# Kernel optimization log

Hardware: AMD Instinct MI355X
Metric: run time of the kernel (lower is better)

The kernel has to match this reference:

```python
import jax, jax.numpy as jnp
import numpy as np

DIM = 1024
HEADS = 16
HEAD_DIM = DIM // HEADS
SCALE = HEAD_DIM ** -0.5


def setup_inputs() -> dict:
    key = jax.random.key(0)
    ks = jax.random.split(key, 8)
    B, Nx, N, C = 4, 2048, 512, DIM
    s = C ** -0.5
    return {
        "x": jax.random.normal(ks[0], (B, Nx, C), jnp.float32),
        "cls": jax.random.normal(ks[1], (B, N, C), jnp.float32),
        # Linear weights stored as [in, out] (y = x @ W); qkv_bias=False so no biases on kv/q/Lin_att
        "w_kv": jax.random.normal(ks[2], (C, 2 * C), jnp.float32) * s,
        "w_q": jax.random.normal(ks[3], (C, C), jnp.float32) * s,
        "w_la": jax.random.normal(ks[4], (C, HEADS), jnp.float32) * s,
        "w_proj": jax.random.normal(ks[5], (C, C), jnp.float32) * s,
        "b_proj": jax.random.normal(ks[6], (C,), jnp.float32) * 0.01,
        "att_weight": jax.random.normal(ks[7], (1,), jnp.float32) * 0.1,
    }


def reference(x, cls, w_kv, w_q, w_la, w_proj, b_proj, att_weight):
    B, N, C = cls.shape
    Nx = x.shape[1]
    H, D = HEADS, C // HEADS

    # kv projection: [B,Nx,2C] -> k,v each [B,H,Nx,D]
    kv = (x @ w_kv).reshape(B, Nx, 2, H, D)
    k = jnp.transpose(kv[:, :, 0], (0, 2, 1, 3))
    v = jnp.transpose(kv[:, :, 1], (0, 2, 1, 3))
    # q projection: [B,H,N,D]
    q = jnp.transpose((cls @ w_q).reshape(B, N, H, D), (0, 2, 1, 3))

    # attention scores and first softmax: [B,H,N,Nx]
    attn = jax.nn.softmax(jnp.einsum("bhnd,bhmd->bhnm", q, k) * SCALE, axis=-1)

    # learned pooled gate: Lin_att(x) -> [B,Nx,H] -> [B,H,Nx] -> pool over tokens
    g = jnp.transpose(x @ w_la, (0, 2, 1))  # [B,H,Nx]
    g_mean = jnp.mean(g, axis=-1)[:, :, None, None]  # [B,H,1,1]
    g_max = jnp.max(g, axis=-1)[:, :, None, None]
    gate = 0.5 * g_mean + 0.5 * g_max

    # second softmax over gated scores, then blend with original attention
    attn2 = jax.nn.softmax(gate * attn, axis=-1)
    w = att_weight[0]
    attn = w * attn2 + (1.0 - w) * attn

    # AV and output projection
    out = jnp.einsum("bhnm,bhmd->bnhd", attn, v).reshape(B, N, C)
    return out @ w_proj + b_proj
```

## Files before the change

kernel.cpp:

```cpp
#include <hip/hip_runtime.h>
#include <stdint.h>

#define NX 2048
#define NQ 512
#define CDIM 1024
#define NH 16
#define DH 64

typedef __attribute__((ext_vector_type(8))) __bf16 bf16x8;
typedef __attribute__((ext_vector_type(4))) float f32x4;

__device__ __forceinline__ uint16_t f2bf(float f) {
  uint32_t i = __float_as_uint(f);
  uint32_t r = i + 0x7fffu + ((i >> 16) & 1u);
  return (uint16_t)(r >> 16);
}

#define GLD16(g, l)                                                            \
  __builtin_amdgcn_global_load_lds(                                            \
      (const __attribute__((address_space(1))) uint32_t*)(g),                  \
      (__attribute__((address_space(3))) uint32_t*)(l), 16, 0, 0)


__global__ __launch_bounds__(256) void cast_bf16_kernel(
    const float* __restrict__ src, uint16_t* __restrict__ dst, int n4) {
  int i = blockIdx.x * blockDim.x + threadIdx.x;
  int stride = gridDim.x * blockDim.x;
  for (; i < n4; i += stride) {
    float4 v = ((const float4*)src)[i];
    ushort4 o;
    o.x = f2bf(v.x); o.y = f2bf(v.y); o.z = f2bf(v.z); o.w = f2bf(v.w);
    ((ushort4*)dst)[i] = o;
  }
}

__global__ __launch_bounds__(256) void transT_bf16_kernel(
    const float* __restrict__ src, uint16_t* __restrict__ dst, int K, int N) {
  __shared__ uint16_t tile[64][65];
  const int k0 = blockIdx.y * 64, n0 = blockIdx.x * 64;
  const int tid = threadIdx.x;
#pragma unroll
  for (int it = 0; it < 16; ++it) {
    int idx = it * 256 + tid;
    int r = idx >> 6, c = idx & 63;
    tile[r][c] = f2bf(src[(size_t)(k0 + r) * N + n0 + c]);
  }
  __syncthreads();
#pragma unroll
  for (int it = 0; it < 16; ++it) {
    int idx = it * 256 + tid;
    int r = idx >> 6, c = idx & 63;
    dst[(size_t)(n0 + r) * K + k0 + c] = tile[c][r];
  }
}


__global__ __launch_bounds__(256) void gate_mm_kernel(
    const uint16_t* __restrict__ xh, const float* __restrict__ wla,
    float* __restrict__ gv) {
  __shared__ __align__(16) uint16_t sW[16 * 1024];
  const int tid = threadIdx.x;
  const int wv = tid >> 6;
  const int lane = tid & 63;
  const int lr = lane & 15;
  const int lh = lane >> 4;

#pragma unroll
  for (int it = 0; it < 64; ++it) {
    int i = it * 256 + tid;
    int c = i >> 4, h = i & 15;
    sW[h * 1024 + (((c >> 3) ^ (h & 7)) << 3) + (c & 7)] = f2bf(wla[i]);
  }
  __syncthreads();

  const int rb = blockIdx.x * 64 + wv * 16;
  f32x4 acc = {0.f, 0.f, 0.f, 0.f};
  for (int t = 0; t < 32; ++t) {
    bf16x8 af = *(const bf16x8*)&xh[(size_t)(rb + lr) * 1024 + t * 32 + lh * 8];
    bf16x8 bf = *(const bf16x8*)&sW[lr * 1024 + (((t * 4 + lh) ^ (lr & 7)) << 3)];
    acc = __builtin_amdgcn_mfma_f32_16x16x32_bf16(af, bf, acc, 0, 0, 0);
  }
  int nxg = rb + lh * 4;
  int b = nxg >> 11, nx = nxg & 2047;
  float4 st = {acc[0], acc[1], acc[2], acc[3]};
  *(float4*)&gv[((size_t)b * NH + lr) * NX + nx] = st;
}


__global__ __launch_bounds__(512, 2) void gemm_kv8(
    const uint16_t* __restrict__ A, const uint16_t* __restrict__ BT,
    uint16_t* __restrict__ outK, uint16_t* __restrict__ outV) {
  __shared__ __align__(16) uint16_t lds[65536];

  const int tid = threadIdx.x;
  const int wid = tid >> 6;
  const int lane = tid & 63;
  const int lr = lane & 15;
  const int lh = lane >> 4;
  const int wm = wid >> 2;
  const int wn = wid & 3;
  const int rowBase = blockIdx.x * 256;
  const int colBase = blockIdx.y * 256;

  f32x4 acc[8][4];
#pragma unroll
  for (int m = 0; m < 8; ++m)
#pragma unroll
    for (int n = 0; n < 4; ++n) acc[m][n] = (f32x4){0.f, 0.f, 0.f, 0.f};

  auto stageB = [&](int T, int h) {
    const uint16_t* srcp = BT + (size_t)(colBase + h * 128) * 1024 + T * 64;
    uint16_t* dst = lds + ((T & 1) * 32768 + 16384 + h * 8192);
#pragma unroll
    for (int it = 0; it < 2; ++it) {
      int s = it * 512 + tid;
      int row = s >> 3, cc = s & 7;
      int sc = cc ^ (row & 7);
      GLD16(srcp + (size_t)row * 1024 + sc * 8,
            dst + ((size_t)it * 512 + wid * 64) * 8);
    }
  };
  auto stageA012 = [&](int T) {
    const uint16_t* srcp = A + (size_t)rowBase * 1024 + T * 64;
    uint16_t* dstbase = lds + (T & 1) * 32768;
    int r64 = tid >> 3, cc = tid & 7;
#pragma unroll
    for (int st = 0; st < 3; ++st) {
      int rloc = (r64 < 32) ? (st * 32 + r64) : (96 + st * 32 + r64);
      int sc = cc ^ (rloc & 7);
      int wrow = (wid < 4) ? (st * 32 + wid * 8) : (128 + st * 32 + (wid - 4) * 8);
      GLD16(srcp + (size_t)rloc * 1024 + sc * 8, dstbase + (size_t)wrow * 64);
    }
  };
  auto stageA3 = [&](int T) {
    const uint16_t* srcp = A + (size_t)rowBase * 1024 + T * 64;
    uint16_t* dstbase = lds + (T & 1) * 32768;
    int r64 = tid >> 3, cc = tid & 7;
    int rloc = (r64 < 32) ? (96 + r64) : (192 + r64);
    int sc = cc ^ (rloc & 7);
    int wrow = (wid < 4) ? (96 + wid * 8) : (224 + (wid - 4) * 8);
    GLD16(srcp + (size_t)rloc * 1024 + sc * 8, dstbase + (size_t)wrow * 64);
  };

  auto rdA = [&](int p, int m, int kk) -> bf16x8 {
    int r = wm * 128 + m * 16 + lr;
    return *(const bf16x8*)&lds[p * 32768 + r * 64 +
                                (((kk * 4 + lh) ^ (r & 7)) << 3)];
  };
  auto rdB = [&](int p, int n, int kk) -> bf16x8 {
    int r = wn * 64 + n * 16 + lr;
    return *(const bf16x8*)&lds[p * 32768 + 16384 + r * 64 +
                                (((kk * 4 + lh) ^ (r & 7)) << 3)];
  };

  auto tile4 = [&](int t, bool last) {
    const int p = t & 1;
    bf16x8 b[4][2], a0[2], a1[2];
#pragma unroll
    for (int q = 0; q < 4; ++q) {
      if (q == 0) {
#pragma unroll
        for (int n = 0; n < 4; ++n)
#pragma unroll
          for (int kk = 0; kk < 2; ++kk) b[n][kk] = rdB(p, n, kk);
      }
#pragma unroll
      for (int kk = 0; kk < 2; ++kk) {
        a0[kk] = rdA(p, 2 * q, kk);
        a1[kk] = rdA(p, 2 * q + 1, kk);
      }
      if (q == 0) {
        stageA3(t + 1);
      } else if (q == 1) {
        if (!last) stageB(t + 2, 0);
      } else if (q == 2) {
        if (!last) stageB(t + 2, 1);
      } else {
        if (!last) stageA012(t + 2);
        if (last)
          asm volatile("s_waitcnt vmcnt(0)" ::: "memory");
        else
          asm volatile("s_waitcnt vmcnt(7)" ::: "memory");
      }
      __builtin_amdgcn_s_barrier();
      asm volatile("s_waitcnt lgkmcnt(0)" ::: "memory");
      __builtin_amdgcn_sched_barrier(0);
      __builtin_amdgcn_s_setprio(1);
#pragma unroll
      for (int n = 0; n < 4; ++n)
#pragma unroll
        for (int kk = 0; kk < 2; ++kk) {
          acc[2 * q][n] = __builtin_amdgcn_mfma_f32_16x16x32_bf16(
              a0[kk], b[n][kk], acc[2 * q][n], 0, 0, 0);
          acc[2 * q + 1][n] = __builtin_amdgcn_mfma_f32_16x16x32_bf16(
              a1[kk], b[n][kk], acc[2 * q + 1][n], 0, 0, 0);
        }
      __builtin_amdgcn_s_setprio(0);
      __builtin_amdgcn_s_barrier();
      asm volatile("" ::: "memory");
    }
  };

  auto tileEpi = [&](int t) {
    const int p = t & 1;
    bf16x8 b[4][2], a0[2], a1[2];
#pragma unroll
    for (int n = 0; n < 4; ++n)
#pragma unroll
      for (int kk = 0; kk < 2; ++kk) b[n][kk] = rdB(p, n, kk);
#pragma unroll
    for (int q = 0; q < 4; ++q) {
#pragma unroll
      for (int kk = 0; kk < 2; ++kk) {
        a0[kk] = rdA(p, 2 * q, kk);
        a1[kk] = rdA(p, 2 * q + 1, kk);
      }
#pragma unroll
      for (int n = 0; n < 4; ++n)
#pragma unroll
        for (int kk = 0; kk < 2; ++kk) {
          acc[2 * q][n] = __builtin_amdgcn_mfma_f32_16x16x32_bf16(
              a0[kk], b[n][kk], acc[2 * q][n], 0, 0, 0);
          acc[2 * q + 1][n] = __builtin_amdgcn_mfma_f32_16x16x32_bf16(
              a1[kk], b[n][kk], acc[2 * q + 1][n], 0, 0, 0);
        }
    }
  };

  stageB(0, 0); stageB(0, 1); stageA012(0); stageA3(0);
  stageB(1, 0); stageB(1, 1); stageA012(1);
  asm volatile("s_waitcnt vmcnt(7)" ::: "memory");
  __builtin_amdgcn_s_barrier();

  for (int t = 0; t < 14; ++t) tile4(t, false);
  tile4(14, true);
  tileEpi(15);

#pragma unroll
  for (int m = 0; m < 8; ++m) {
    int gr0 = rowBase + wm * 128 + m * 16 + lh * 4;
    int b_ = gr0 >> 11, nx0 = gr0 & 2047;
#pragma unroll
    for (int n = 0; n < 4; ++n) {
      int gc = colBase + wn * 64 + n * 16 + lr;
      if (gc < 1024) {
        int hh = gc >> 6, d = gc & 63;
        size_t base = (((size_t)b_ * NH + hh) * NX + nx0) * DH + d;
#pragma unroll
        for (int j = 0; j < 4; ++j)
          outK[base + (size_t)j * DH] = f2bf(acc[m][n][j]);
      } else {
        int c2 = gc - 1024;
        int hh = c2 >> 6, d = c2 & 63;
        ushort4 pv;
        pv.x = f2bf(acc[m][n][0]);
        pv.y = f2bf(acc[m][n][1]);
        pv.z = f2bf(acc[m][n][2]);
        pv.w = f2bf(acc[m][n][3]);
        *(ushort4*)&outV[(((size_t)b_ * NH + hh) * DH + d) * NX + nx0] = pv;
      }
    }
  }
}


template <int MODE>
__global__ __launch_bounds__(256) void gemm_bt(
    const uint16_t* __restrict__ A, const uint16_t* __restrict__ BT,
    uint16_t* __restrict__ outA, uint16_t* __restrict__ outB,
    float* __restrict__ outF, const float* __restrict__ bias) {
  constexpr int K = 1024;
  __shared__ __align__(16) uint16_t sA[128 * 32];
  __shared__ __align__(16) uint16_t sB[128 * 32];

  const int tid = threadIdx.x;
  const int wv = tid >> 6;
  const int lane = tid & 63;
  const int lr = lane & 15;
  const int lh = lane >> 4;
  const int wm = wv >> 1, wn = wv & 1;
  const int rowBase = blockIdx.x * 128;
  const int colBase = blockIdx.y * 128;

  f32x4 zero4 = {0.f, 0.f, 0.f, 0.f};
  f32x4 acc[4][4];
#pragma unroll
  for (int m = 0; m < 4; ++m)
#pragma unroll
    for (int n = 0; n < 4; ++n) acc[m][n] = zero4;

  for (int k0 = 0; k0 < K; k0 += 32) {
#pragma unroll
    for (int it = 0; it < 2; ++it) {
      int s = it * 256 + tid;
      int row = s >> 2, cc = s & 3;
      int sc = cc ^ ((row >> 1) & 3);
      GLD16(A + (size_t)(rowBase + row) * K + k0 + sc * 8,
            sA + ((size_t)it * 256 + wv * 64) * 8);
      GLD16(BT + (size_t)(colBase + row) * K + k0 + sc * 8,
            sB + ((size_t)it * 256 + wv * 64) * 8);
    }
    __syncthreads();
    bf16x8 af[4], bfr[4];
#pragma unroll
    for (int m = 0; m < 4; ++m) {
      int r = wm * 64 + m * 16 + lr;
      af[m] = *(const bf16x8*)&sA[r * 32 + ((lh ^ ((r >> 1) & 3)) << 3)];
    }
#pragma unroll
    for (int n = 0; n < 4; ++n) {
      int r = wn * 64 + n * 16 + lr;
      bfr[n] = *(const bf16x8*)&sB[r * 32 + ((lh ^ ((r >> 1) & 3)) << 3)];
    }
#pragma unroll
    for (int m = 0; m < 4; ++m)
#pragma unroll
      for (int n = 0; n < 4; ++n)
        acc[m][n] = __builtin_amdgcn_mfma_f32_16x16x32_bf16(af[m], bfr[n],
                                                            acc[m][n], 0, 0, 0);
    __syncthreads();
  }

#pragma unroll
  for (int m = 0; m < 4; ++m) {
    int gr0 = rowBase + wm * 64 + m * 16 + lh * 4;
#pragma unroll
    for (int n = 0; n < 4; ++n) {
      int gc = colBase + wn * 64 + n * 16 + lr;
      if (MODE == 1) {
        int b = gr0 >> 9, nq0 = gr0 & 511;
        int hh = gc >> 6, d = gc & 63;
        size_t base = (((size_t)b * NH + hh) * NQ + nq0) * DH + d;
#pragma unroll
        for (int j = 0; j < 4; ++j)
          outA[base + (size_t)j * DH] = f2bf(acc[m][n][j] * 0.125f);
      } else {
        float bi = bias[gc];
#pragma unroll
        for (int j = 0; j < 4; ++j)
          outF[(size_t)(gr0 + j) * 1024 + gc] = acc[m][n][j] + bi;
      }
    }
  }
}


__global__ __launch_bounds__(256) void gate2_kernel(
    const float* __restrict__ gv, float* __restrict__ gate) {
  const int bh = blockIdx.x;
  const int tid = threadIdx.x;
  const float* p = gv + (size_t)bh * NX;
  float s = 0.f, mx = -1e30f;
  for (int i = tid; i < NX; i += 256) {
    float v = p[i];
    s += v;
    mx = fmaxf(mx, v);
  }
#pragma unroll
  for (int off = 1; off < 64; off <<= 1) {
    s += __shfl_xor(s, off, 64);
    mx = fmaxf(mx, __shfl_xor(mx, off, 64));
  }
  __shared__ float ss[4], sm[4];
  int wv = tid >> 6, lane = tid & 63;
  if (lane == 0) { ss[wv] = s; sm[wv] = mx; }
  __syncthreads();
  if (tid == 0) {
    float S = ss[0] + ss[1] + ss[2] + ss[3];
    float M = fmaxf(fmaxf(sm[0], sm[1]), fmaxf(sm[2], sm[3]));
    gate[bh] = 0.5f * (S / (float)NX) + 0.5f * M;
  }
}


__global__ __launch_bounds__(256) void vcolsum_kernel(
    const uint16_t* __restrict__ VT, float* __restrict__ vcs) {
  const int bh = blockIdx.x;
  const int wv = threadIdx.x >> 6, lane = threadIdx.x & 63;
#pragma unroll
  for (int dd = 0; dd < 16; ++dd) {
    int d = dd * 4 + wv;
    const uint16_t* row = VT + ((size_t)bh * DH + d) * NX;
    float s = 0.f;
#pragma unroll
    for (int i = 0; i < 4; ++i) {
      bf16x8 v = *(const bf16x8*)&row[(i * 64 + lane) * 8];
#pragma unroll
      for (int j = 0; j < 8; ++j) s += (float)v[j];
    }
#pragma unroll
    for (int off = 1; off < 64; off <<= 1) s += __shfl_xor(s, off, 64);
    if (lane == 0) vcs[bh * DH + d] = s;
  }
}


__global__ __launch_bounds__(256) void attn_kernel(
    const uint16_t* __restrict__ Q, const uint16_t* __restrict__ K,
    const uint16_t* __restrict__ VT, const float* __restrict__ gate,
    const float* __restrict__ attw, const float* __restrict__ vcs,
    uint16_t* __restrict__ ctxh) {
  __shared__ __align__(16) uint16_t sK[128 * 64];
  __shared__ __align__(16) uint16_t sV[64 * 128];
  __shared__ __align__(16) __bf16 sPe[64 * 128];

  const int tid = threadIdx.x;
  const int wv = tid >> 6;
  const int lane = tid & 63;
  const int lr = lane & 15;
  const int lh = lane >> 4;
  const int bh = blockIdx.x;
  const int q0 = blockIdx.y * 64;
  const float g = gate[bh];
  const float w = attw[0];

  const uint16_t* Qb = Q + ((size_t)bh * NQ + q0) * DH;
  const uint16_t* Kb = K + (size_t)bh * NX * DH;
  const uint16_t* Vb = VT + (size_t)bh * DH * NX;

  bf16x8 qa[2];
#pragma unroll
  for (int kk = 0; kk < 2; ++kk)
    qa[kk] = *(const bf16x8*)&Qb[(wv * 16 + lr) * DH + kk * 32 + lh * 8];

  float lp[4] = {0.f, 0.f, 0.f, 0.f};
  f32x4 zero4 = {0.f, 0.f, 0.f, 0.f};
  f32x4 accp[4];
#pragma unroll
  for (int d = 0; d < 4; ++d) accp[d] = zero4;

  for (int kt = 0; kt < 16; ++kt) {
#pragma unroll
    for (int it = 0; it < 4; ++it) {
      int s = it * 256 + tid;
      int row = s >> 3, cc = s & 7;
      int sc = cc ^ (row & 7);
      GLD16(Kb + (size_t)(kt * 128 + row) * DH + sc * 8,
            sK + ((size_t)it * 256 + wv * 64) * 8);
    }
#pragma unroll
    for (int it = 0; it < 4; ++it) {
      int s = it * 256 + tid;
      int row = s >> 4, cc = s & 15;
      int sc = cc ^ (row & 15);
      GLD16(Vb + (size_t)row * NX + kt * 128 + sc * 8,
            sV + ((size_t)it * 256 + wv * 64) * 8);
    }
    __syncthreads();
#pragma unroll
    for (int n = 0; n < 8; ++n) {
      f32x4 a4 = {0.f, 0.f, 0.f, 0.f};
      int r = n * 16 + lr;
#pragma unroll
      for (int kk = 0; kk < 2; ++kk) {
        bf16x8 kb = *(const bf16x8*)&sK[r * 64 + (((kk * 4 + lh) ^ (r & 7)) << 3)];
        a4 = __builtin_amdgcn_mfma_f32_16x16x32_bf16(qa[kk], kb, a4, 0, 0, 0);
      }
#pragma unroll
      for (int j = 0; j < 4; ++j) {
        float e = __expf(a4[j]);
        lp[j] += e;
        int qr = wv * 16 + lh * 4 + j;
        int key = n * 16 + lr;
        int idx = qr * 128 + ((((key >> 3) ^ (qr & 15))) << 3) + (key & 7);
        sPe[idx] = (__bf16)e;
      }
    }
    __syncthreads();
    const int prow = wv * 16 + lr;
#pragma unroll
    for (int kk = 0; kk < 4; ++kk) {
      int pidx = prow * 128 + (((kk * 4 + lh) ^ (prow & 15)) << 3);
      bf16x8 pe = *(const bf16x8*)&sPe[pidx];
#pragma unroll
      for (int df = 0; df < 4; ++df) {
        int vr = df * 16 + lr;
        bf16x8 vb = *(const bf16x8*)&sV[vr * 128 + (((kk * 4 + lh) ^ (vr & 15)) << 3)];
        accp[df] = __builtin_amdgcn_mfma_f32_16x16x32_bf16(pe, vb, accp[df], 0, 0, 0);
      }
    }
    __syncthreads();
  }
#pragma unroll
  for (int off = 1; off < 16; off <<= 1)
#pragma unroll
    for (int j = 0; j < 4; ++j) lp[j] += __shfl_xor(lp[j], off, 64);

  const int b = bh >> 4, h = bh & 15;
  const float c1 = w / ((float)NX + g);
  const float c2 = w * g / ((float)NX + g) + (1.f - w);
  float rl[4];
#pragma unroll
  for (int j = 0; j < 4; ++j) rl[j] = 1.f / lp[j];
#pragma unroll
  for (int df = 0; df < 4; ++df) {
    int d = df * 16 + lr;
    float cv = vcs[bh * DH + d];
#pragma unroll
    for (int j = 0; j < 4; ++j) {
      int qr = q0 + wv * 16 + lh * 4 + j;
      float p = accp[df][j] * rl[j];
      ctxh[(((size_t)b * NQ + qr) * NH + h) * DH + d] = f2bf(c1 * cv + c2 * p);
    }
  }
}


extern "C" void kernel_launch(void* const* d_in, const int* in_sizes, int n_in,
                              void* d_out, int out_size, void* d_ws,
                              size_t ws_size, hipStream_t stream) {
  const float* x = (const float*)d_in[0];
  const float* cls = (const float*)d_in[1];
  const float* w_kv = (const float*)d_in[2];
  const float* w_q = (const float*)d_in[3];
  const float* w_la = (const float*)d_in[4];
  const float* w_proj = (const float*)d_in[5];
  const float* b_proj = (const float*)d_in[6];
  const float* att_w = (const float*)d_in[7];
  float* out = (float*)d_out;

  char* ws = (char*)d_ws;
  size_t off = 0;
  auto alloc = [&](size_t bytes) {
    void* p = ws + off;
    off += (bytes + 255) & ~(size_t)255;
    return p;
  };
  uint16_t* xh = (uint16_t*)alloc(4ull * NX * CDIM * 2);
  uint16_t* ch = (uint16_t*)alloc(4ull * NQ * CDIM * 2);
  uint16_t* wkvT = (uint16_t*)alloc(2048ull * 1024 * 2);
  uint16_t* wqT = (uint16_t*)alloc(1024ull * 1024 * 2);
  uint16_t* wpT = (uint16_t*)alloc(1024ull * 1024 * 2);
  uint16_t* kbf = (uint16_t*)alloc(4ull * NH * NX * DH * 2);
  uint16_t* vT = (uint16_t*)alloc(4ull * NH * DH * NX * 2);
  uint16_t* qbf = (uint16_t*)alloc(4ull * NH * NQ * DH * 2);
  float* gv = (float*)alloc(4ull * NH * NX * 4);
  float* gate = (float*)alloc(1024);
  float* vcs = (float*)alloc(4ull * NH * DH * 4);
  uint16_t* ctxh = (uint16_t*)alloc(4ull * NQ * CDIM * 2);

  cast_bf16_kernel<<<2048, 256, 0, stream>>>(x, xh, 4 * NX * CDIM / 4);
  cast_bf16_kernel<<<1024, 256, 0, stream>>>(cls, ch, 4 * NQ * CDIM / 4);
  transT_bf16_kernel<<<dim3(32, 16), 256, 0, stream>>>(w_kv, wkvT, 1024, 2048);
  transT_bf16_kernel<<<dim3(16, 16), 256, 0, stream>>>(w_q, wqT, 1024, 1024);
  transT_bf16_kernel<<<dim3(16, 16), 256, 0, stream>>>(w_proj, wpT, 1024, 1024);

  gate_mm_kernel<<<128, 256, 0, stream>>>(xh, w_la, gv);
  gemm_kv8<<<dim3(32, 8), 512, 0, stream>>>(xh, wkvT, kbf, vT);
  gemm_bt<1><<<dim3(16, 8), 256, 0, stream>>>(ch, wqT, qbf, nullptr, nullptr, nullptr);

  gate2_kernel<<<64, 256, 0, stream>>>(gv, gate);
  vcolsum_kernel<<<64, 256, 0, stream>>>(vT, vcs);

  attn_kernel<<<dim3(64, 8), 256, 0, stream>>>(qbf, kbf, vT, gate, att_w, vcs, ctxh);

  gemm_bt<2><<<dim3(16, 8), 256, 0, stream>>>(ctxh, wpT, nullptr, nullptr, out, b_proj);
}
```

Measured before the change: 161.7 us.

## Merge cast, transpose and Q projection launches into fewer kernels

The two fp32-to-bf16 casts become one kernel, and the three weight transposes become one launch indexed by blockIdx.z. The Q projection now runs inside the large KV GEMM kernel as extra blocks, so it shares that kernel's pipelined 256x256 tile path and the grid fills more of the device. The V column-sum kernel is split over a second grid axis to get more parallel blocks. The aim is to cut launch count and fill underused GPU waves, at the cost of idle blocks (early returns in the transpose and Q tiles) and more branching in the merged kernels.

```diff
diff --git a/kernel.cpp b/kernel.cpp
--- a/kernel.cpp
+++ b/kernel.cpp
@@ -22,22 +22,43 @@
       (__attribute__((address_space(3))) uint32_t*)(l), 16, 0, 0)
 
 
-__global__ __launch_bounds__(256) void cast_bf16_kernel(
-    const float* __restrict__ src, uint16_t* __restrict__ dst, int n4) {
+__global__ __launch_bounds__(256) void cast2_bf16_kernel(
+    const float* __restrict__ s0, uint16_t* __restrict__ d0, int n40,
+    const float* __restrict__ s1, uint16_t* __restrict__ d1, int n41) {
   int i = blockIdx.x * blockDim.x + threadIdx.x;
   int stride = gridDim.x * blockDim.x;
-  for (; i < n4; i += stride) {
-    float4 v = ((const float4*)src)[i];
-    ushort4 o;
-    o.x = f2bf(v.x); o.y = f2bf(v.y); o.z = f2bf(v.z); o.w = f2bf(v.w);
-    ((ushort4*)dst)[i] = o;
-  }
-}
-
-__global__ __launch_bounds__(256) void transT_bf16_kernel(
-    const float* __restrict__ src, uint16_t* __restrict__ dst, int K, int N) {
+  int ntot = n40 + n41;
+  for (; i < ntot; i += stride) {
+    if (i < n40) {
+      float4 v = ((const float4*)s0)[i];
+      ushort4 o;
+      o.x = f2bf(v.x); o.y = f2bf(v.y); o.z = f2bf(v.z); o.w = f2bf(v.w);
+      ((ushort4*)d0)[i] = o;
+    } else {
+      float4 v = ((const float4*)s1)[i - n40];
+      ushort4 o;
+      o.x = f2bf(v.x); o.y = f2bf(v.y); o.z = f2bf(v.z); o.w = f2bf(v.w);
+      ((ushort4*)d1)[i - n40] = o;
+    }
+  }
+}
+
+
+__global__ __launch_bounds__(256) void transT_all_kernel(
+    const float* __restrict__ w_kv, uint16_t* __restrict__ wkvT,
+    const float* __restrict__ w_q, uint16_t* __restrict__ wqT,
+    const float* __restrict__ w_proj, uint16_t* __restrict__ wpT) {
+  const int z = blockIdx.z;
+  const float* src;
+  uint16_t* dst;
+  int N;
+  if (z == 0) { src = w_kv; dst = wkvT; N = 2048; }
+  else if (z == 1) { src = w_q; dst = wqT; N = 1024; }
+  else { src = w_proj; dst = wpT; N = 1024; }
+  const int n0 = blockIdx.x * 64;
+  if (n0 >= N) return;
+  const int k0 = blockIdx.y * 64;
   __shared__ uint16_t tile[64][65];
-  const int k0 = blockIdx.y * 64, n0 = blockIdx.x * 64;
   const int tid = threadIdx.x;
 #pragma unroll
   for (int it = 0; it < 16; ++it) {
@@ -50,7 +71,7 @@
   for (int it = 0; it < 16; ++it) {
     int idx = it * 256 + tid;
     int r = idx >> 6, c = idx & 63;
-    dst[(size_t)(n0 + r) * K + k0 + c] = tile[c][r];
+    dst[(size_t)(n0 + r) * 1024 + k0 + c] = tile[c][r];
   }
 }
 
@@ -87,10 +108,21 @@
 }
 
 
-__global__ __launch_bounds__(512, 2) void gemm_kv8(
+__global__ __launch_bounds__(512, 2) void gemm_kv8q(
     const uint16_t* __restrict__ A, const uint16_t* __restrict__ BT,
-    uint16_t* __restrict__ outK, uint16_t* __restrict__ outV) {
+    uint16_t* __restrict__ outK, uint16_t* __restrict__ outV,
+    const uint16_t* __restrict__ Aq, const uint16_t* __restrict__ BTq,
+    uint16_t* __restrict__ outQ) {
   __shared__ __align__(16) uint16_t lds[65536];
+
+  const int bx = blockIdx.x, by = blockIdx.y;
+  const bool isQ = bx >= 32;
+  if (isQ && by >= 4) return;
+
+  const uint16_t* Ap = isQ ? Aq : A;
+  const uint16_t* BTp = isQ ? BTq : BT;
+  const int rowBase = (isQ ? (bx - 32) : bx) * 256;
+  const int colBase = by * 256;
 
   const int tid = threadIdx.x;
   const int wid = tid >> 6;
@@ -99,8 +131,6 @@
   const int lh = lane >> 4;
   const int wm = wid >> 2;
   const int wn = wid & 3;
-  const int rowBase = blockIdx.x * 256;
-  const int colBase = blockIdx.y * 256;
 
   f32x4 acc[8][4];
 #pragma unroll
@@ -109,7 +139,7 @@
     for (int n = 0; n < 4; ++n) acc[m][n] = (f32x4){0.f, 0.f, 0.f, 0.f};
 
   auto stageB = [&](int T, int h) {
-    const uint16_t* srcp = BT + (size_t)(colBase + h * 128) * 1024 + T * 64;
+    const uint16_t* srcp = BTp + (size_t)(colBase + h * 128) * 1024 + T * 64;
     uint16_t* dst = lds + ((T & 1) * 32768 + 16384 + h * 8192);
 #pragma unroll
     for (int it = 0; it < 2; ++it) {
@@ -121,7 +151,7 @@
     }
   };
   auto stageA012 = [&](int T) {
-    const uint16_t* srcp = A + (size_t)rowBase * 1024 + T * 64;
+    const uint16_t* srcp = Ap + (size_t)rowBase * 1024 + T * 64;
     uint16_t* dstbase = lds + (T & 1) * 32768;
     int r64 = tid >> 3, cc = tid & 7;
 #pragma unroll
@@ -133,7 +163,7 @@
     }
   };
   auto stageA3 = [&](int T) {
-    const uint16_t* srcp = A + (size_t)rowBase * 1024 + T * 64;
+    const uint16_t* srcp = Ap + (size_t)rowBase * 1024 + T * 64;
     uint16_t* dstbase = lds + (T & 1) * 32768;
     int r64 = tid >> 3, cc = tid & 7;
     int rloc = (r64 < 32) ? (96 + r64) : (192 + r64);
@@ -236,38 +266,53 @@
   tile4(14, true);
   tileEpi(15);
 
-#pragma unroll
-  for (int m = 0; m < 8; ++m) {
-    int gr0 = rowBase + wm * 128 + m * 16 + lh * 4;
-    int b_ = gr0 >> 11, nx0 = gr0 & 2047;
-#pragma unroll
-    for (int n = 0; n < 4; ++n) {
-      int gc = colBase + wn * 64 + n * 16 + lr;
-      if (gc < 1024) {
+  if (isQ) {
+#pragma unroll
+    for (int m = 0; m < 8; ++m) {
+      int gr0 = rowBase + wm * 128 + m * 16 + lh * 4;
+      int b_ = gr0 >> 9, nq0 = gr0 & 511;
+#pragma unroll
+      for (int n = 0; n < 4; ++n) {
+        int gc = colBase + wn * 64 + n * 16 + lr;
         int hh = gc >> 6, d = gc & 63;
-        size_t base = (((size_t)b_ * NH + hh) * NX + nx0) * DH + d;
+        size_t base = (((size_t)b_ * NH + hh) * NQ + nq0) * DH + d;
 #pragma unroll
         for (int j = 0; j < 4; ++j)
-          outK[base + (size_t)j * DH] = f2bf(acc[m][n][j]);
-      } else {
-        int c2 = gc - 1024;
-        int hh = c2 >> 6, d = c2 & 63;
-        ushort4 pv;
-        pv.x = f2bf(acc[m][n][0]);
-        pv.y = f2bf(acc[m][n][1]);
-        pv.z = f2bf(acc[m][n][2]);
-        pv.w = f2bf(acc[m][n][3]);
-        *(ushort4*)&outV[(((size_t)b_ * NH + hh) * DH + d) * NX + nx0] = pv;
-      }
-    }
-  }
-}
-
-
-template <int MODE>
-__global__ __launch_bounds__(256) void gemm_bt(
+          outQ[base + (size_t)j * DH] = f2bf(acc[m][n][j] * 0.125f);
+      }
+    }
+  } else {
+#pragma unroll
+    for (int m = 0; m < 8; ++m) {
+      int gr0 = rowBase + wm * 128 + m * 16 + lh * 4;
+      int b_ = gr0 >> 11, nx0 = gr0 & 2047;
+#pragma unroll
+      for (int n = 0; n < 4; ++n) {
+        int gc = colBase + wn * 64 + n * 16 + lr;
+        if (gc < 1024) {
+          int hh = gc >> 6, d = gc & 63;
+          size_t base = (((size_t)b_ * NH + hh) * NX + nx0) * DH + d;
+#pragma unroll
+          for (int j = 0; j < 4; ++j)
+            outK[base + (size_t)j * DH] = f2bf(acc[m][n][j]);
+        } else {
+          int c2 = gc - 1024;
+          int hh = c2 >> 6, d = c2 & 63;
+          ushort4 pv;
+          pv.x = f2bf(acc[m][n][0]);
+          pv.y = f2bf(acc[m][n][1]);
+          pv.z = f2bf(acc[m][n][2]);
+          pv.w = f2bf(acc[m][n][3]);
+          *(ushort4*)&outV[(((size_t)b_ * NH + hh) * DH + d) * NX + nx0] = pv;
+        }
+      }
+    }
+  }
+}
+
+
+__global__ __launch_bounds__(256) void gemm_proj(
     const uint16_t* __restrict__ A, const uint16_t* __restrict__ BT,
-    uint16_t* __restrict__ outA, uint16_t* __restrict__ outB,
     float* __restrict__ outF, const float* __restrict__ bias) {
   constexpr int K = 1024;
   __shared__ __align__(16) uint16_t sA[128 * 32];
@@ -327,19 +372,10 @@
 #pragma unroll
     for (int n = 0; n < 4; ++n) {
       int gc = colBase + wn * 64 + n * 16 + lr;
-      if (MODE == 1) {
-        int b = gr0 >> 9, nq0 = gr0 & 511;
-        int hh = gc >> 6, d = gc & 63;
-        size_t base = (((size_t)b * NH + hh) * NQ + nq0) * DH + d;
-#pragma unroll
-        for (int j = 0; j < 4; ++j)
-          outA[base + (size_t)j * DH] = f2bf(acc[m][n][j] * 0.125f);
-      } else {
-        float bi = bias[gc];
-#pragma unroll
-        for (int j = 0; j < 4; ++j)
-          outF[(size_t)(gr0 + j) * 1024 + gc] = acc[m][n][j] + bi;
-      }
+      float bi = bias[gc];
+#pragma unroll
+      for (int j = 0; j < 4; ++j)
+        outF[(size_t)(gr0 + j) * 1024 + gc] = acc[m][n][j] + bi;
     }
   }
 }
@@ -378,8 +414,8 @@
   const int bh = blockIdx.x;
   const int wv = threadIdx.x >> 6, lane = threadIdx.x & 63;
 #pragma unroll
-  for (int dd = 0; dd < 16; ++dd) {
-    int d = dd * 4 + wv;
+  for (int dd = 0; dd < 4; ++dd) {
+    int d = blockIdx.y * 16 + dd * 4 + wv;
     const uint16_t* row = VT + ((size_t)bh * DH + d) * NX;
     float s = 0.f;
 #pragma unroll
@@ -539,20 +575,18 @@
   float* vcs = (float*)alloc(4ull * NH * DH * 4);
   uint16_t* ctxh = (uint16_t*)alloc(4ull * NQ * CDIM * 2);
 
-  cast_bf16_kernel<<<2048, 256, 0, stream>>>(x, xh, 4 * NX * CDIM / 4);
-  cast_bf16_kernel<<<1024, 256, 0, stream>>>(cls, ch, 4 * NQ * CDIM / 4);
-  transT_bf16_kernel<<<dim3(32, 16), 256, 0, stream>>>(w_kv, wkvT, 1024, 2048);
-  transT_bf16_kernel<<<dim3(16, 16), 256, 0, stream>>>(w_q, wqT, 1024, 1024);
-  transT_bf16_kernel<<<dim3(16, 16), 256, 0, stream>>>(w_proj, wpT, 1024, 1024);
+  cast2_bf16_kernel<<<2048, 256, 0, stream>>>(x, xh, 4 * NX * CDIM / 4,
+                                              cls, ch, 4 * NQ * CDIM / 4);
+  transT_all_kernel<<<dim3(32, 16, 3), 256, 0, stream>>>(w_kv, wkvT, w_q, wqT,
+                                                         w_proj, wpT);
 
   gate_mm_kernel<<<128, 256, 0, stream>>>(xh, w_la, gv);
-  gemm_kv8<<<dim3(32, 8), 512, 0, stream>>>(xh, wkvT, kbf, vT);
-  gemm_bt<1><<<dim3(16, 8), 256, 0, stream>>>(ch, wqT, qbf, nullptr, nullptr, nullptr);
+  gemm_kv8q<<<dim3(40, 8), 512, 0, stream>>>(xh, wkvT, kbf, vT, ch, wqT, qbf);
 
   gate2_kernel<<<64, 256, 0, stream>>>(gv, gate);
-  vcolsum_kernel<<<64, 256, 0, stream>>>(vT, vcs);
+  vcolsum_kernel<<<dim3(64, 4), 256, 0, stream>>>(vT, vcs);
 
   attn_kernel<<<dim3(64, 8), 256, 0, stream>>>(qbf, kbf, vT, gate, att_w, vcs, ctxh);
 
-  gemm_bt<2><<<dim3(16, 8), 256, 0, stream>>>(ctxh, wpT, nullptr, nullptr, out, b_proj);
-}
+  gemm_proj<<<dim3(16, 8), 256, 0, stream>>>(ctxh, wpT, out, b_proj);
+}
```

Measured after the change: 157.8 us. 2.4% less time.
